# Kernel tuning notes

Measured on AMD Instinct MI355X. Metric: run time of the kernel, lower is better.

Reference implementation:

```python
import jax, jax.numpy as jnp
import numpy as np

B, T, N, F, H, K, E = 4, 256, 48, 4, 64, 4, 192
LH, C = 512, 8
NEG_SLOPE = 0.2


def setup_inputs() -> dict:
    key = jax.random.key(0)
    ks = jax.random.split(key, 16)
    rn = lambda k, shape, s=0.1: jax.random.normal(k, shape, jnp.float32) * s
    x = jax.random.normal(ks[0], (B, T, N, F), jnp.float32)
    edge_index = jax.random.randint(ks[1], (2, E), 0, N, jnp.int32)
    return dict(
        x=x,
        edge_index=edge_index,
        # GATv2 layer 1: F -> K*H, concat heads
        Wl1=rn(ks[2], (F, K * H)), Wr1=rn(ks[3], (F, K * H)),
        att1=rn(ks[4], (K, H)), b1=rn(ks[5], (K * H,)),
        # GATv2 layer 2: K*H -> H, mean over heads
        Wl2=rn(ks[6], (K * H, K * H)), Wr2=rn(ks[7], (K * H, K * H)),
        att2=rn(ks[8], (K, H)), b2=rn(ks[9], (H,)),
        # LSTM (torch gate order i,f,g,o)
        W_ih=rn(ks[10], (4 * LH, N * H), 0.02), W_hh=rn(ks[11], (4 * LH, LH), 0.02),
        b_ih=rn(ks[12], (4 * LH,), 0.02), b_hh=rn(ks[13], (4 * LH,), 0.02),
        fc_w=rn(ks[14], (C, LH)), fc_b=rn(ks[15], (C,)),
    )


def gatv2(xn, src, dst, Wl, Wr, att, bias, concat):
    # xn: [G, N, Fin]; shared edge list src/dst: [E]
    G = xn.shape[0]
    xl = (xn @ Wl).reshape(G, N, K, H)  # source transform (messages)
    xr = (xn @ Wr).reshape(G, N, K, H)  # target transform
    s = jax.nn.leaky_relu(xl[:, src] + xr[:, dst], NEG_SLOPE)  # [G,E,K,H]
    e = jnp.einsum('gekh,kh->gek', s, att)                      # [G,E,K]
    seg_max = jax.vmap(lambda v: jax.ops.segment_max(v, dst, num_segments=N))(e)  # [G,N,K]
    p = jnp.exp(e - seg_max[:, dst])
    denom = jax.vmap(lambda v: jax.ops.segment_sum(v, dst, num_segments=N))(p)
    alpha = p / (denom[:, dst] + 1e-16)                         # softmax over in-edges per node
    msg = alpha[..., None] * xl[:, src]                         # [G,E,K,H]
    out = jax.vmap(lambda m: jax.ops.segment_sum(m, dst, num_segments=N))(msg)  # [G,N,K,H]
    out = out.reshape(G, N, K * H) if concat else out.mean(axis=2)
    return out + bias


def lstm_last(seq, W_ih, W_hh, b_ih, b_hh):
    # seq: [B, T, In] -> last hidden state [B, LH]
    xw = jnp.einsum('bti,gi->btg', seq, W_ih) + (b_ih + b_hh)  # precompute input part
    def step(carry, xt):
        h, c = carry
        g = xt + h @ W_hh.T
        i, f, gg, o = jnp.split(g, 4, axis=-1)
        c = jax.nn.sigmoid(f) * c + jax.nn.sigmoid(i) * jnp.tanh(gg)
        h = jax.nn.sigmoid(o) * jnp.tanh(c)
        return (h, c), None
    h0 = jnp.zeros((seq.shape[0], LH), seq.dtype)
    (h, _c), _ = jax.lax.scan(step, (h0, h0), jnp.swapaxes(xw, 0, 1))
    return h


def reference(x, edge_index, Wl1, Wr1, att1, b1, Wl2, Wr2, att2, b2,
              W_ih, W_hh, b_ih, b_hh, fc_w, fc_b):
    src, dst = edge_index[0], edge_index[1]
    xg = x.reshape(B * T, N, F)
    h1 = jax.nn.relu(gatv2(xg, src, dst, Wl1, Wr1, att1, b1, True))   # [G,N,K*H]
    h2 = jax.nn.relu(gatv2(h1, src, dst, Wl2, Wr2, att2, b2, False))  # [G,N,H]
    seq = h2.reshape(B, T, N * H)
    hT = lstm_last(seq, W_ih, W_hh, b_ih, b_hh)
    return hT @ fc_w.T + fc_b  # [B, C]
```

## Files before the change

kernel.cpp:

```cpp
#include <hip/hip_runtime.h>
#include <math.h>

typedef unsigned short u16;
typedef unsigned int u32;
typedef unsigned long long u64;

#define NB 4
#define NT 256
#define NN 48
#define NF 4
#define NH 64
#define NK 4
#define NE 192
#define NLH 512
#define NC 8
#define NG 1024
#define KH 256
#define SEQD 3072
#define G4 2048
#define LSTM_NBLK 64

typedef __attribute__((ext_vector_type(8))) short bf16x8;
typedef __attribute__((ext_vector_type(4))) float f32x4;

__device__ __forceinline__ float bf2f(u16 v) {
  union { u32 u; float f; } c; c.u = ((u32)v) << 16; return c.f;
}
__device__ __forceinline__ u16 f2bf(float f) {
  union { float f; u32 u; } c; c.f = f;
  u32 r = c.u + 0x7FFFu + ((c.u >> 16) & 1u);
  return (u16)(r >> 16);
}
__device__ __forceinline__ u32 fbits(float f) { union { float f; u32 u; } c; c.f = f; return c.u; }
__device__ __forceinline__ float bitsf(u32 u) { union { u32 u; float f; } c; c.u = u; return c.f; }

__global__ void setup_kernel(const int* __restrict__ ei, int* __restrict__ coff,
                             int* __restrict__ ceid)
{
  if (threadIdx.x == 0 && blockIdx.x == 0) {
    int cnt[NN];
    for (int n = 0; n < NN; ++n) cnt[n] = 0;
    for (int e = 0; e < NE; ++e) cnt[ei[NE + e]]++;
    coff[0] = 0;
    for (int n = 0; n < NN; ++n) coff[n + 1] = coff[n] + cnt[n];
    int pos[NN];
    for (int n = 0; n < NN; ++n) pos[n] = coff[n];
    for (int e = 0; e < NE; ++e) { int d = ei[NE + e]; ceid[pos[d]++] = e; }
  }
}

__global__ void wtc_kernel(const float* __restrict__ Wl2, const float* __restrict__ Wr2,
                           u16* __restrict__ WTc)
{
  int id0 = blockIdx.x * 256 + threadIdx.x;
#pragma unroll
  for (int rep = 0; rep < 4; ++rep) {
    int id = id0 + rep * 32768;
    int n = id >> 8, k = id & 255;
    float v = (n < 256) ? Wl2[k * 256 + n] : Wr2[k * 256 + (n - 256)];
    WTc[id] = f2bf(v);
  }
}

__global__ void wihb_kernel(const float* __restrict__ Wih, u16* __restrict__ WihB)
{
  int id = (blockIdx.x * 256 + threadIdx.x) * 8;
  float4 a = *(const float4*)(Wih + id);
  float4 b = *(const float4*)(Wih + id + 4);
  u16* dst = WihB + id;
  dst[0] = f2bf(a.x); dst[1] = f2bf(a.y); dst[2] = f2bf(a.z); dst[3] = f2bf(a.w);
  dst[4] = f2bf(b.x); dst[5] = f2bf(b.y); dst[6] = f2bf(b.z); dst[7] = f2bf(b.w);
}

__global__ __launch_bounds__(256) void gat_fused_kernel(
    const float* __restrict__ x, const int* __restrict__ ei,
    const int* __restrict__ coff, const int* __restrict__ ceid,
    const float* __restrict__ Wl1, const float* __restrict__ Wr1,
    const float* __restrict__ att1, const float* __restrict__ b1,
    const u16* __restrict__ WTc,
    const float* __restrict__ att2, const float* __restrict__ b2,
    u16* __restrict__ h2b)
{
  __shared__ u16 xlds[NN * 512];
  __shared__ float sWl1[NF * KH], sWr1[NF * KH];
  __shared__ float satt[KH];
  __shared__ float sbias[KH];
  __shared__ float sx[NN * NF];
  __shared__ float esc[NE * NK];
  __shared__ int soff[NN + 1];
  __shared__ u16 seid[NE], ssrc[NE], sdst[NE];

  const int tid = threadIdx.x;
  const int g = blockIdx.x;
  const int lane = tid & 63, wv = tid >> 6;
  const int l15 = lane & 15, q = lane >> 4;

#pragma unroll
  for (int rep = 0; rep < 4; ++rep) {
    int idx = rep * 256 + tid;
    sWl1[idx] = Wl1[idx];
    sWr1[idx] = Wr1[idx];
  }
  satt[tid] = att1[tid];
  sbias[tid] = b1[tid];
  if (tid < NN * NF) sx[tid] = x[(size_t)g * (NN * NF) + tid];
  if (tid < NE) {
    ssrc[tid] = (u16)ei[tid];
    sdst[tid] = (u16)ei[NE + tid];
    seid[tid] = (u16)ceid[tid];
  }
  if (tid < NN + 1) soff[tid] = coff[tid];
  __syncthreads();

  {
    float w0 = sWl1[tid], w1 = sWl1[256 + tid], w2 = sWl1[512 + tid], w3 = sWl1[768 + tid];
    float v0 = sWr1[tid], v1 = sWr1[256 + tid], v2 = sWr1[512 + tid], v3 = sWr1[768 + tid];
#pragma unroll 4
    for (int n = 0; n < NN; ++n) {
      float x0 = sx[n * 4 + 0], x1 = sx[n * 4 + 1], x2 = sx[n * 4 + 2], x3 = sx[n * 4 + 3];
      float xl = fmaf(x3, w3, fmaf(x2, w2, fmaf(x1, w1, x0 * w0)));
      float xr = fmaf(x3, v3, fmaf(x2, v2, fmaf(x1, v1, x0 * v0)));
      xlds[n * 512 + tid] = f2bf(xl);
      xlds[n * 512 + 256 + tid] = f2bf(xr);
    }
  }
  __syncthreads();

  for (int task = tid; task < NE * NK; task += 256) {
    int e = task >> 2, k = task & 3;
    int s = ssrc[e], d = sdst[e];
    const u16* xls = xlds + s * 512 + k * 64;
    const u16* xrd = xlds + d * 512 + 256 + k * 64;
    const float* ap = satt + k * 64;
    float acc = 0.f;
    for (int h = 0; h < 64; ++h) {
      float tv = bf2f(xls[h]) + bf2f(xrd[h]);
      tv = tv > 0.f ? tv : 0.2f * tv;
      acc = fmaf(tv, ap[h], acc);
    }
    esc[e * 4 + k] = acc;
  }
  __syncthreads();

  if (tid < NN * NK) {
    int n = tid >> 2, k = tid & 3;
    int e0 = soff[n], e1 = soff[n + 1];
    if (e1 > e0) {
      float m = -1e30f;
      for (int j = e0; j < e1; ++j) m = fmaxf(m, esc[seid[j] * 4 + k]);
      float den = 0.f;
      for (int j = e0; j < e1; ++j) {
        float pv = expf(esc[seid[j] * 4 + k] - m);
        esc[seid[j] * 4 + k] = pv;
        den += pv;
      }
      float inv = 1.f / (den + 1e-16f);
      for (int j = e0; j < e1; ++j) esc[seid[j] * 4 + k] *= inv;
    }
  }
  __syncthreads();

  satt[tid] = att2[tid];
  {
    int o = tid, k = o >> 6;
    for (int n = 0; n < NN; ++n) {
      int e0 = soff[n], e1 = soff[n + 1];
      float acc = 0.f;
      for (int j = e0; j < e1; ++j) {
        int e = seid[j];
        int s = ssrc[e];
        acc = fmaf(esc[e * 4 + k], bf2f(xlds[s * 512 + o]), acc);
      }
      float ov = acc + sbias[o];
      xlds[n * 512 + 256 + o] = f2bf(fmaxf(ov, 0.f));
    }
  }
  __syncthreads();
  if (tid < NH) sbias[tid] = b2[tid];

  bf16x8 afr[3][8];
#pragma unroll
  for (int mt = 0; mt < 3; ++mt)
#pragma unroll
    for (int kt = 0; kt < 8; ++kt)
      afr[mt][kt] = *(const bf16x8*)(xlds + (mt * 16 + l15) * 512 + 256 + kt * 32 + q * 8);
  __syncthreads();

#pragma unroll
  for (int t = 0; t < 8; ++t) {
    int n0 = (wv * 8 + t) * 16;
    const u16* bcol = WTc + (size_t)(n0 + l15) * KH + q * 8;
    f32x4 acc0 = {0.f, 0.f, 0.f, 0.f}, acc1 = acc0, acc2 = acc0;
#pragma unroll
    for (int kt = 0; kt < 8; ++kt) {
      bf16x8 bfr = *(const bf16x8*)(bcol + kt * 32);
      acc0 = __builtin_amdgcn_mfma_f32_16x16x32_bf16(afr[0][kt], bfr, acc0, 0, 0, 0);
      acc1 = __builtin_amdgcn_mfma_f32_16x16x32_bf16(afr[1][kt], bfr, acc1, 0, 0, 0);
      acc2 = __builtin_amdgcn_mfma_f32_16x16x32_bf16(afr[2][kt], bfr, acc2, 0, 0, 0);
    }
#pragma unroll
    for (int r = 0; r < 4; ++r) {
      int rw = q * 4 + r;
      xlds[(0 * 16 + rw) * 512 + n0 + l15] = f2bf(acc0[r]);
      xlds[(1 * 16 + rw) * 512 + n0 + l15] = f2bf(acc1[r]);
      xlds[(2 * 16 + rw) * 512 + n0 + l15] = f2bf(acc2[r]);
    }
  }
  __syncthreads();

  for (int task = tid; task < NE * NK; task += 256) {
    int e = task >> 2, k = task & 3;
    int s = ssrc[e], d = sdst[e];
    const u16* xls = xlds + s * 512 + k * 64;
    const u16* xrd = xlds + d * 512 + 256 + k * 64;
    const float* ap = satt + k * 64;
    float acc = 0.f;
    for (int h = 0; h < 64; ++h) {
      float tv = bf2f(xls[h]) + bf2f(xrd[h]);
      tv = tv > 0.f ? tv : 0.2f * tv;
      acc = fmaf(tv, ap[h], acc);
    }
    esc[e * 4 + k] = acc;
  }
  __syncthreads();

  if (tid < NN * NK) {
    int n = tid >> 2, k = tid & 3;
    int e0 = soff[n], e1 = soff[n + 1];
    if (e1 > e0) {
      float m = -1e30f;
      for (int j = e0; j < e1; ++j) m = fmaxf(m, esc[seid[j] * 4 + k]);
      float den = 0.f;
      for (int j = e0; j < e1; ++j) {
        float pv = expf(esc[seid[j] * 4 + k] - m);
        esc[seid[j] * 4 + k] = pv;
        den += pv;
      }
      float inv = 1.f / (den + 1e-16f);
      for (int j = e0; j < e1; ++j) esc[seid[j] * 4 + k] *= inv;
    }
  }
  __syncthreads();

  for (int task = tid; task < NN * NH; task += 256) {
    int n = task >> 6, h = task & 63;
    int e0 = soff[n], e1 = soff[n + 1];
    float acc = 0.f;
    for (int j = e0; j < e1; ++j) {
      int e = seid[j];
      int s = ssrc[e];
      const u16* xls = xlds + s * 512 + h;
#pragma unroll
      for (int k = 0; k < 4; ++k)
        acc = fmaf(esc[e * 4 + k], bf2f(xls[k * 64]), acc);
    }
    float ov = fmaf(acc, 0.25f, sbias[h]);
    h2b[(size_t)g * SEQD + task] = f2bf(fmaxf(ov, 0.f));
  }
}

__global__ __launch_bounds__(256) void xw_mfma_kernel(const u16* __restrict__ h2b,
                                                      const u16* __restrict__ WihB,
                                                      const float* __restrict__ bih,
                                                      const float* __restrict__ bhh,
                                                      float* __restrict__ xw)
{
  const int tid = threadIdx.x, lane = tid & 63, wv = tid >> 6;
  const int l15 = lane & 15, q = lane >> 4;
  const int gt = blockIdx.x & 15, rt = blockIdx.x >> 4;
  const int g0 = gt * 64, r0 = rt * 128;

  const u16* arow[4];
#pragma unroll
  for (int mt = 0; mt < 4; ++mt)
    arow[mt] = h2b + (size_t)(g0 + mt * 16 + l15) * SEQD + q * 8;
  const u16* brow[2];
  int ncol[2];
#pragma unroll
  for (int tn = 0; tn < 2; ++tn) {
    ncol[tn] = r0 + (wv * 2 + tn) * 16 + l15;
    brow[tn] = WihB + (size_t)ncol[tn] * SEQD + q * 8;
  }

  f32x4 acc[4][2];
#pragma unroll
  for (int mt = 0; mt < 4; ++mt)
#pragma unroll
    for (int tn = 0; tn < 2; ++tn) acc[mt][tn] = (f32x4){0.f, 0.f, 0.f, 0.f};

  for (int kt = 0; kt < SEQD / 32; ++kt) {
    bf16x8 af[4], bfv[2];
#pragma unroll
    for (int mt = 0; mt < 4; ++mt) af[mt] = *(const bf16x8*)(arow[mt] + kt * 32);
#pragma unroll
    for (int tn = 0; tn < 2; ++tn) bfv[tn] = *(const bf16x8*)(brow[tn] + kt * 32);
#pragma unroll
    for (int mt = 0; mt < 4; ++mt)
#pragma unroll
      for (int tn = 0; tn < 2; ++tn)
        acc[mt][tn] = __builtin_amdgcn_mfma_f32_16x16x32_bf16(af[mt], bfv[tn], acc[mt][tn], 0, 0, 0);
  }

#pragma unroll
  for (int tn = 0; tn < 2; ++tn) {
    float bias = bih[ncol[tn]] + bhh[ncol[tn]];
#pragma unroll
    for (int mt = 0; mt < 4; ++mt)
#pragma unroll
      for (int r = 0; r < 4; ++r) {
        int gg = g0 + mt * 16 + q * 4 + r;
        xw[(size_t)gg * G4 + ncol[tn]] = acc[mt][tn][r] + bias;
      }
  }
}

__global__ __launch_bounds__(256) void lstm_kernel(const float* __restrict__ xw,
                                                   const float* __restrict__ Whh,
                                                   const float* __restrict__ fcw,
                                                   const float* __restrict__ fcb,
                                                   u64* pairs,
                                                   float* __restrict__ out)
{
  __shared__ float hlds[NB * NLH];
  __shared__ float part[2][8][32][4];
  __shared__ float clds[8][4];
  __shared__ float fcpart[32][8];

  const int tid = threadIdx.x;
  const int blk = blockIdx.x;
  const int r32 = tid & 31, p = tid >> 5;
  const int lane = tid & 63, w = tid >> 6;
  const int R = (r32 >> 3) * NLH + blk * 8 + (r32 & 7);

  float wreg[64];
  {
    const float4* wsrc = (const float4*)(Whh + (size_t)R * NLH + p * 64);
#pragma unroll
    for (int q = 0; q < 16; ++q) {
      float4 v = wsrc[q];
      wreg[4 * q + 0] = v.x; wreg[4 * q + 1] = v.y;
      wreg[4 * q + 2] = v.z; wreg[4 * q + 3] = v.w;
    }
  }
  if (tid < 32) {
    int u = tid & 7, b = tid >> 3;
    clds[u][b] = 0.f;
    __hip_atomic_store(&pairs[0 * (NB * NLH) + b * NLH + blk * 8 + u], 0ULL,
                       __ATOMIC_RELAXED, __HIP_MEMORY_SCOPE_AGENT);
  }

  for (int s = 0; s < NT; ++s) {
    float myxw[4];
    if (tid < 32) {
      int u = tid & 7, b = tid >> 3;
#pragma unroll
      for (int G = 0; G < 4; ++G)
        myxw[G] = xw[(size_t)(b * NT + s) * G4 + G * 512 + blk * 8 + u];
    }
    {
      u64* pb = pairs + (size_t)(s & 1) * (NB * NLH);
      const int u0 = w * 128 + lane, u1 = u0 + 64;
      u64 v[8];
      while (true) {
#pragma unroll
        for (int b = 0; b < NB; ++b) {
          v[2 * b]     = __hip_atomic_load(&pb[b * NLH + u0],
                                           __ATOMIC_RELAXED, __HIP_MEMORY_SCOPE_AGENT);
          v[2 * b + 1] = __hip_atomic_load(&pb[b * NLH + u1],
                                           __ATOMIC_RELAXED, __HIP_MEMORY_SCOPE_AGENT);
        }
        int mn = 0x7fffffff;
#pragma unroll
        for (int q = 0; q < 8; ++q) mn = min(mn, (int)(u32)(v[q] >> 32));
        if (__all(mn >= s)) break;
      }
#pragma unroll
      for (int b = 0; b < NB; ++b) {
        hlds[b * NLH + u0] = bitsf((u32)v[2 * b]);
        hlds[b * NLH + u1] = bitsf((u32)v[2 * b + 1]);
      }
    }

    float a0 = 0.f, a1 = 0.f, a2 = 0.f, a3 = 0.f;
    const float* h0 = &hlds[0 * NLH + p * 64];
    const float* h1p = &hlds[1 * NLH + p * 64];
    const float* h2p = &hlds[2 * NLH + p * 64];
    const float* h3p = &hlds[3 * NLH + p * 64];
#pragma unroll
    for (int j = 0; j < 16; ++j) {
      float w0 = wreg[4 * j], w1 = wreg[4 * j + 1], w2 = wreg[4 * j + 2], w3 = wreg[4 * j + 3];
      float4 v0 = *(const float4*)(h0 + 4 * j);
      float4 v1 = *(const float4*)(h1p + 4 * j);
      float4 v2 = *(const float4*)(h2p + 4 * j);
      float4 v3 = *(const float4*)(h3p + 4 * j);
      a0 = fmaf(v0.w, w3, fmaf(v0.z, w2, fmaf(v0.y, w1, fmaf(v0.x, w0, a0))));
      a1 = fmaf(v1.w, w3, fmaf(v1.z, w2, fmaf(v1.y, w1, fmaf(v1.x, w0, a1))));
      a2 = fmaf(v2.w, w3, fmaf(v2.z, w2, fmaf(v2.y, w1, fmaf(v2.x, w0, a2))));
      a3 = fmaf(v3.w, w3, fmaf(v3.z, w2, fmaf(v3.y, w1, fmaf(v3.x, w0, a3))));
    }
    float (*pt)[32][4] = part[s & 1];
    pt[p][r32][0] = a0; pt[p][r32][1] = a1;
    pt[p][r32][2] = a2; pt[p][r32][3] = a3;
    __syncthreads();
    if (tid < 32) {
      int u = tid & 7, b = tid >> 3;
      float gsum[4];
#pragma unroll
      for (int G = 0; G < 4; ++G) {
        float t = myxw[G];
#pragma unroll
        for (int pp = 0; pp < 8; ++pp) t += pt[pp][G * 8 + u][b];
        gsum[G] = t;
      }
      float si = 1.f / (1.f + expf(-gsum[0]));
      float sf = 1.f / (1.f + expf(-gsum[1]));
      float so = 1.f / (1.f + expf(-gsum[3]));
      float cn = fmaf(sf, clds[u][b], si * tanhf(gsum[2]));
      float hn = so * tanhf(cn);
      clds[u][b] = cn;
      u64 pk = ((u64)(u32)(s + 1) << 32) | (u64)fbits(hn);
      __hip_atomic_store(&pairs[(size_t)((s + 1) & 1) * (NB * NLH) + b * NLH + blk * 8 + u],
                         pk, __ATOMIC_RELAXED, __HIP_MEMORY_SCOPE_AGENT);
    }
  }

  if (blk == 0) {
    {
      u64* pb = pairs + (size_t)(NT & 1) * (NB * NLH);
      const int u0 = w * 128 + lane, u1 = u0 + 64;
      u64 v[8];
      while (true) {
#pragma unroll
        for (int b = 0; b < NB; ++b) {
          v[2 * b]     = __hip_atomic_load(&pb[b * NLH + u0],
                                           __ATOMIC_RELAXED, __HIP_MEMORY_SCOPE_AGENT);
          v[2 * b + 1] = __hip_atomic_load(&pb[b * NLH + u1],
                                           __ATOMIC_RELAXED, __HIP_MEMORY_SCOPE_AGENT);
        }
        int mn = 0x7fffffff;
#pragma unroll
        for (int q = 0; q < 8; ++q) mn = min(mn, (int)(u32)(v[q] >> 32));
        if (__all(mn >= NT)) break;
      }
#pragma unroll
      for (int b = 0; b < NB; ++b) {
        hlds[b * NLH + u0] = bitsf((u32)v[2 * b]);
        hlds[b * NLH + u1] = bitsf((u32)v[2 * b + 1]);
      }
    }
    __syncthreads();
    int pr = tid >> 3, l = tid & 7;
    int b = pr >> 3, cc = pr & 7;
    const float* hf = hlds + b * NLH;
    float a = 0.f;
    int base = cc * NLH + l * 64;
    for (int j = 0; j < 64; ++j) a = fmaf(hf[l * 64 + j], fcw[base + j], a);
    fcpart[pr][l] = a;
    __syncthreads();
    if (tid < 32) {
      float s = fcb[tid & 7];
#pragma unroll
      for (int l2 = 0; l2 < 8; ++l2) s += fcpart[tid][l2];
      out[tid] = s;
    }
  }
}

extern "C" void kernel_launch(void* const* d_in, const int* in_sizes, int n_in,
                              void* d_out, int out_size, void* d_ws, size_t ws_size,
                              hipStream_t stream)
{
  (void)in_sizes; (void)n_in; (void)out_size; (void)ws_size;
  const float* x    = (const float*)d_in[0];
  const int*   ei   = (const int*)d_in[1];
  const float* Wl1  = (const float*)d_in[2];
  const float* Wr1  = (const float*)d_in[3];
  const float* att1 = (const float*)d_in[4];
  const float* b1   = (const float*)d_in[5];
  const float* Wl2  = (const float*)d_in[6];
  const float* Wr2  = (const float*)d_in[7];
  const float* att2 = (const float*)d_in[8];
  const float* b2   = (const float*)d_in[9];
  const float* Wih  = (const float*)d_in[10];
  const float* Whh  = (const float*)d_in[11];
  const float* bih  = (const float*)d_in[12];
  const float* bhh  = (const float*)d_in[13];
  const float* fcw  = (const float*)d_in[14];
  const float* fcb  = (const float*)d_in[15];

  char* ws = (char*)d_ws;
  int* csr_off = (int*)(ws + 0);
  int* csr_eid = (int*)(ws + 256);
  u64* pairs   = (u64*)(ws + 1024);
  u16* WTc     = (u16*)(ws + 40960);
  u16* WihB    = (u16*)(ws + 303104);
  u16* h2b     = (u16*)(ws + 12886016);
  float* xwb   = (float*)(ws + 19177472);
  float* outp  = (float*)d_out;

  setup_kernel<<<1, 64, 0, stream>>>(ei, csr_off, csr_eid);
  wtc_kernel<<<128, 256, 0, stream>>>(Wl2, Wr2, WTc);
  wihb_kernel<<<3072, 256, 0, stream>>>(Wih, WihB);
  gat_fused_kernel<<<NG, 256, 0, stream>>>(x, ei, csr_off, csr_eid,
                                           Wl1, Wr1, att1, b1,
                                           WTc, att2, b2, h2b);
  xw_mfma_kernel<<<256, 256, 0, stream>>>(h2b, WihB, bih, bhh, xwb);
  lstm_kernel<<<LSTM_NBLK, 256, 0, stream>>>(xwb, Whh, fcw, fcb, pairs, outp);
}
```

Before: 1.252 ms.

## Restructure LSTM recurrence into 256 single-wave blocks with poison-flag history buffer

The persistent LSTM kernel now runs as 256 single-wavefront blocks, each owning 2 hidden units, instead of 64 blocks of 256 threads. Partial dot products are reduced with wave shuffles rather than a shared-memory partial array. Step-to-step synchronisation moves from a double-buffered (step, value) pair array to a per-step history buffer. A fill kernel pre-poisons that buffer so readiness is detected by non-NaN-poison values, with two h values packed per 64-bit store. Fast exp-based sigmoid/tanh replace the library calls, which trades some accuracy. The history buffer reuses the h2b workspace region after it has been consumed, which relies on kernel ordering and requires all 256 blocks to be co-resident.

Result: slower. 1.440 ms (+15.0%).

```diff
diff --git a/kernel.cpp b/kernel.cpp
--- a/kernel.cpp
+++ b/kernel.cpp
@@ -18,7 +18,8 @@
 #define KH 256
 #define SEQD 3072
 #define G4 2048
-#define LSTM_NBLK 64
+
+#define POISON 0x7FC000ADu
 
 typedef __attribute__((ext_vector_type(8))) short bf16x8;
 typedef __attribute__((ext_vector_type(4))) float f32x4;
@@ -33,6 +34,16 @@
 }
 __device__ __forceinline__ u32 fbits(float f) { union { float f; u32 u; } c; c.f = f; return c.u; }
 __device__ __forceinline__ float bitsf(u32 u) { union { u32 u; float f; } c; c.u = u; return c.f; }
+
+__device__ __forceinline__ float sigm_fast(float x) {
+  return 1.f / (1.f + __expf(-x));
+}
+__device__ __forceinline__ float tanh_fast(float x) {
+  float ax = fabsf(x);
+  float t = __expf(-2.f * ax);
+  float r = (1.f - t) / (1.f + t);
+  return x < 0.f ? -r : r;
+}
 
 __global__ void setup_kernel(const int* __restrict__ ei, int* __restrict__ coff,
                              int* __restrict__ ceid)
@@ -70,6 +81,14 @@
   u16* dst = WihB + id;
   dst[0] = f2bf(a.x); dst[1] = f2bf(a.y); dst[2] = f2bf(a.z); dst[3] = f2bf(a.w);
   dst[4] = f2bf(b.x); dst[5] = f2bf(b.y); dst[6] = f2bf(b.z); dst[7] = f2bf(b.w);
+}
+
+__global__ void fill_kernel(u32* __restrict__ buf)
+{
+  int id = blockIdx.x * 256 + threadIdx.x;
+  u32 v = (id < 512) ? 0u : POISON;
+  uint4 q = make_uint4(v, v, v, v);
+  ((uint4*)buf)[id] = q;
 }
 
 __global__ __launch_bounds__(256) void gat_fused_kernel(
@@ -314,27 +333,24 @@
   }
 }
 
-__global__ __launch_bounds__(256) void lstm_kernel(const float* __restrict__ xw,
-                                                   const float* __restrict__ Whh,
-                                                   const float* __restrict__ fcw,
-                                                   const float* __restrict__ fcb,
-                                                   u64* pairs,
-                                                   float* __restrict__ out)
-{
-  __shared__ float hlds[NB * NLH];
-  __shared__ float part[2][8][32][4];
-  __shared__ float clds[8][4];
-  __shared__ float fcpart[32][8];
-
-  const int tid = threadIdx.x;
+__global__ __launch_bounds__(64) void lstm_wave_kernel(
+    const float* __restrict__ xw, const float* __restrict__ Whh,
+    const float* __restrict__ fcw, const float* __restrict__ fcb,
+    u32* buf, float* __restrict__ out)
+{
+  __shared__ float hbuf[4 * 544];
+  __shared__ float gl[32];
+
+  const int lane = threadIdx.x;
   const int blk = blockIdx.x;
-  const int r32 = tid & 31, p = tid >> 5;
-  const int lane = tid & 63, w = tid >> 6;
-  const int R = (r32 >> 3) * NLH + blk * 8 + (r32 & 7);
+  const int rl = lane >> 3;
+  const int ck = lane & 7;
+  const int G = rl >> 1, ul = rl & 1;
+  const int row = G * NLH + blk * 2 + ul;
 
   float wreg[64];
   {
-    const float4* wsrc = (const float4*)(Whh + (size_t)R * NLH + p * 64);
+    const float4* wsrc = (const float4*)(Whh + (size_t)row * NLH + ck * 64);
 #pragma unroll
     for (int q = 0; q < 16; ++q) {
       float4 v = wsrc[q];
@@ -342,54 +358,50 @@
       wreg[4 * q + 2] = v.z; wreg[4 * q + 3] = v.w;
     }
   }
-  if (tid < 32) {
-    int u = tid & 7, b = tid >> 3;
-    clds[u][b] = 0.f;
-    __hip_atomic_store(&pairs[0 * (NB * NLH) + b * NLH + blk * 8 + u], 0ULL,
-                       __ATOMIC_RELAXED, __HIP_MEMORY_SCOPE_AGENT);
-  }
+
+  const int fu = lane >> 2, fb = lane & 3;
+  const int cb = lane >> 5, lj = (lane & 31) * 2;
+  float creg = 0.f;
 
   for (int s = 0; s < NT; ++s) {
     float myxw[4];
-    if (tid < 32) {
-      int u = tid & 7, b = tid >> 3;
-#pragma unroll
-      for (int G = 0; G < 4; ++G)
-        myxw[G] = xw[(size_t)(b * NT + s) * G4 + G * 512 + blk * 8 + u];
-    }
-    {
-      u64* pb = pairs + (size_t)(s & 1) * (NB * NLH);
-      const int u0 = w * 128 + lane, u1 = u0 + 64;
-      u64 v[8];
-      while (true) {
-#pragma unroll
-        for (int b = 0; b < NB; ++b) {
-          v[2 * b]     = __hip_atomic_load(&pb[b * NLH + u0],
-                                           __ATOMIC_RELAXED, __HIP_MEMORY_SCOPE_AGENT);
-          v[2 * b + 1] = __hip_atomic_load(&pb[b * NLH + u1],
-                                           __ATOMIC_RELAXED, __HIP_MEMORY_SCOPE_AGENT);
-        }
-        int mn = 0x7fffffff;
-#pragma unroll
-        for (int q = 0; q < 8; ++q) mn = min(mn, (int)(u32)(v[q] >> 32));
-        if (__all(mn >= s)) break;
-      }
-#pragma unroll
-      for (int b = 0; b < NB; ++b) {
-        hlds[b * NLH + u0] = bitsf((u32)v[2 * b]);
-        hlds[b * NLH + u1] = bitsf((u32)v[2 * b + 1]);
-      }
-    }
+    if (lane < 8) {
+      int un = blk * 2 + fu;
+#pragma unroll
+      for (int g2 = 0; g2 < 4; ++g2)
+        myxw[g2] = xw[(size_t)(fb * NT + s) * G4 + g2 * NLH + un];
+    }
+
+    const u64* pb = (const u64*)(buf + (size_t)s * 2048);
+    u64 v[16];
+    while (true) {
+#pragma unroll
+      for (int k = 0; k < 16; ++k)
+        v[k] = __hip_atomic_load(&pb[k * 64 + lane],
+                                 __ATOMIC_RELAXED, __HIP_MEMORY_SCOPE_AGENT);
+      int ok = 1;
+#pragma unroll
+      for (int k = 0; k < 16; ++k)
+        ok &= ((u32)v[k] != POISON) && ((u32)(v[k] >> 32) != POISON);
+      if (__all(ok)) break;
+    }
+
+#pragma unroll
+    for (int k = 0; k < 16; ++k) {
+      union { u64 u; float2 f; } cv; cv.u = v[k];
+      *(float2*)(hbuf + (k >> 2) * 544 + ((k & 3) * 2 + cb) * 68 + lj) = cv.f;
+    }
+    __syncthreads();
 
     float a0 = 0.f, a1 = 0.f, a2 = 0.f, a3 = 0.f;
-    const float* h0 = &hlds[0 * NLH + p * 64];
-    const float* h1p = &hlds[1 * NLH + p * 64];
-    const float* h2p = &hlds[2 * NLH + p * 64];
-    const float* h3p = &hlds[3 * NLH + p * 64];
+    const float* h0p = hbuf + 0 * 544 + ck * 68;
+    const float* h1p = hbuf + 1 * 544 + ck * 68;
+    const float* h2p = hbuf + 2 * 544 + ck * 68;
+    const float* h3p = hbuf + 3 * 544 + ck * 68;
 #pragma unroll
     for (int j = 0; j < 16; ++j) {
       float w0 = wreg[4 * j], w1 = wreg[4 * j + 1], w2 = wreg[4 * j + 2], w3 = wreg[4 * j + 3];
-      float4 v0 = *(const float4*)(h0 + 4 * j);
+      float4 v0 = *(const float4*)(h0p + 4 * j);
       float4 v1 = *(const float4*)(h1p + 4 * j);
       float4 v2 = *(const float4*)(h2p + 4 * j);
       float4 v3 = *(const float4*)(h3p + 4 * j);
@@ -398,71 +410,76 @@
       a2 = fmaf(v2.w, w3, fmaf(v2.z, w2, fmaf(v2.y, w1, fmaf(v2.x, w0, a2))));
       a3 = fmaf(v3.w, w3, fmaf(v3.z, w2, fmaf(v3.y, w1, fmaf(v3.x, w0, a3))));
     }
-    float (*pt)[32][4] = part[s & 1];
-    pt[p][r32][0] = a0; pt[p][r32][1] = a1;
-    pt[p][r32][2] = a2; pt[p][r32][3] = a3;
+
+#pragma unroll
+    for (int m = 1; m <= 4; m <<= 1) {
+      a0 += __shfl_xor(a0, m);
+      a1 += __shfl_xor(a1, m);
+      a2 += __shfl_xor(a2, m);
+      a3 += __shfl_xor(a3, m);
+    }
+    if (ck < 4) {
+      float sv = a0;
+      sv = (ck == 1) ? a1 : sv;
+      sv = (ck == 2) ? a2 : sv;
+      sv = (ck == 3) ? a3 : sv;
+      gl[rl * 4 + ck] = sv;
+    }
     __syncthreads();
-    if (tid < 32) {
-      int u = tid & 7, b = tid >> 3;
-      float gsum[4];
-#pragma unroll
-      for (int G = 0; G < 4; ++G) {
-        float t = myxw[G];
-#pragma unroll
-        for (int pp = 0; pp < 8; ++pp) t += pt[pp][G * 8 + u][b];
-        gsum[G] = t;
+
+    if (lane < 8) {
+      float gi = gl[(0 * 2 + fu) * 4 + fb] + myxw[0];
+      float gf = gl[(1 * 2 + fu) * 4 + fb] + myxw[1];
+      float gg = gl[(2 * 2 + fu) * 4 + fb] + myxw[2];
+      float go = gl[(3 * 2 + fu) * 4 + fb] + myxw[3];
+      float cn = fmaf(sigm_fast(gf), creg, sigm_fast(gi) * tanh_fast(gg));
+      creg = cn;
+      float hn = sigm_fast(go) * tanh_fast(cn);
+      u32 hb = fbits(hn);
+      if (hb == POISON) hb ^= 1u;
+      u32 other = (u32)__shfl((int)hb, lane + 4);
+      if (fu == 0) {
+        u64 pk = (u64)hb | ((u64)other << 32);
+        u64* dst = (u64*)(buf + (size_t)(s + 1) * 2048 + fb * NLH + blk * 2);
+        __hip_atomic_store(dst, pk, __ATOMIC_RELAXED, __HIP_MEMORY_SCOPE_AGENT);
       }
-      float si = 1.f / (1.f + expf(-gsum[0]));
-      float sf = 1.f / (1.f + expf(-gsum[1]));
-      float so = 1.f / (1.f + expf(-gsum[3]));
-      float cn = fmaf(sf, clds[u][b], si * tanhf(gsum[2]));
-      float hn = so * tanhf(cn);
-      clds[u][b] = cn;
-      u64 pk = ((u64)(u32)(s + 1) << 32) | (u64)fbits(hn);
-      __hip_atomic_store(&pairs[(size_t)((s + 1) & 1) * (NB * NLH) + b * NLH + blk * 8 + u],
-                         pk, __ATOMIC_RELAXED, __HIP_MEMORY_SCOPE_AGENT);
     }
   }
 
   if (blk == 0) {
-    {
-      u64* pb = pairs + (size_t)(NT & 1) * (NB * NLH);
-      const int u0 = w * 128 + lane, u1 = u0 + 64;
-      u64 v[8];
-      while (true) {
-#pragma unroll
-        for (int b = 0; b < NB; ++b) {
-          v[2 * b]     = __hip_atomic_load(&pb[b * NLH + u0],
-                                           __ATOMIC_RELAXED, __HIP_MEMORY_SCOPE_AGENT);
-          v[2 * b + 1] = __hip_atomic_load(&pb[b * NLH + u1],
-                                           __ATOMIC_RELAXED, __HIP_MEMORY_SCOPE_AGENT);
-        }
-        int mn = 0x7fffffff;
-#pragma unroll
-        for (int q = 0; q < 8; ++q) mn = min(mn, (int)(u32)(v[q] >> 32));
-        if (__all(mn >= NT)) break;
-      }
-#pragma unroll
-      for (int b = 0; b < NB; ++b) {
-        hlds[b * NLH + u0] = bitsf((u32)v[2 * b]);
-        hlds[b * NLH + u1] = bitsf((u32)v[2 * b + 1]);
-      }
+    const u64* pb = (const u64*)(buf + (size_t)NT * 2048);
+    u64 v[16];
+    while (true) {
+#pragma unroll
+      for (int k = 0; k < 16; ++k)
+        v[k] = __hip_atomic_load(&pb[k * 64 + lane],
+                                 __ATOMIC_RELAXED, __HIP_MEMORY_SCOPE_AGENT);
+      int ok = 1;
+#pragma unroll
+      for (int k = 0; k < 16; ++k)
+        ok &= ((u32)v[k] != POISON) && ((u32)(v[k] >> 32) != POISON);
+      if (__all(ok)) break;
+    }
+#pragma unroll
+    for (int k = 0; k < 16; ++k) {
+      union { u64 u; float2 f; } cv; cv.u = v[k];
+      *(float2*)(hbuf + (k >> 2) * 544 + ((k & 3) * 2 + cb) * 68 + lj) = cv.f;
     }
     __syncthreads();
-    int pr = tid >> 3, l = tid & 7;
-    int b = pr >> 3, cc = pr & 7;
-    const float* hf = hlds + b * NLH;
+    const int task = lane >> 1, half = lane & 1;
+    const int b = task >> 3, c = task & 7;
+    const float* wrow = fcw + c * NLH + half * 256;
+    const float* hrow = hbuf + b * 544 + half * 4 * 68;
     float a = 0.f;
-    int base = cc * NLH + l * 64;
-    for (int j = 0; j < 64; ++j) a = fmaf(hf[l * 64 + j], fcw[base + j], a);
-    fcpart[pr][l] = a;
-    __syncthreads();
-    if (tid < 32) {
-      float s = fcb[tid & 7];
-#pragma unroll
-      for (int l2 = 0; l2 < 8; ++l2) s += fcpart[tid][l2];
-      out[tid] = s;
-    }
+#pragma unroll
+    for (int j = 0; j < 64; ++j) {
+      int u = 4 * j;
+      float4 wv = *(const float4*)(wrow + u);
+      float4 hv = *(const float4*)(hrow + (u >> 6) * 68 + (u & 63));
+      a = fmaf(hv.w, wv.w, fmaf(hv.z, wv.z, fmaf(hv.y, wv.y, fmaf(hv.x, wv.x, a))));
+    }
+    a += __shfl_xor(a, 1);
+    if (half == 0) out[task] = a + fcb[c];
   }
 }
 
@@ -491,10 +508,10 @@
   char* ws = (char*)d_ws;
   int* csr_off = (int*)(ws + 0);
   int* csr_eid = (int*)(ws + 256);
-  u64* pairs   = (u64*)(ws + 1024);
   u16* WTc     = (u16*)(ws + 40960);
   u16* WihB    = (u16*)(ws + 303104);
   u16* h2b     = (u16*)(ws + 12886016);
+  u32* bufp    = (u32*)(ws + 12886016);
   float* xwb   = (float*)(ws + 19177472);
   float* outp  = (float*)d_out;
 
@@ -505,5 +522,6 @@
                                            Wl1, Wr1, att1, b1,
                                            WTc, att2, b2, h2b);
   xw_mfma_kernel<<<256, 256, 0, stream>>>(h2b, WihB, bih, bhh, xwb);
-  lstm_kernel<<<LSTM_NBLK, 256, 0, stream>>>(xwb, Whh, fcw, fcb, pairs, outp);
-}
+  fill_kernel<<<514, 256, 0, stream>>>(bufp);
+  lstm_wave_kernel<<<256, 64, 0, stream>>>(xwb, Whh, fcw, fcb, bufp, outp);
+}
```
